# Kernel optimization log

Measured on AMD Instinct MI355X. Metric: run time of the kernel, lower is better.

The kernel has to match this reference:

```python
import jax, jax.numpy as jnp
import numpy as np
import math

D_MODEL = 1024
D_STATE = 16
D_CONV = 4
EXPAND = 2
D_INNER = EXPAND * D_MODEL
DT_RANK = max(D_MODEL // 16, 1)
B_SZ, L_SEQ = 2, 2048
DT_MIN, DT_MAX = 1e-3, 1e-1


def setup_inputs() -> dict:
    key = jax.random.key(0)
    ks = jax.random.split(key, 10)
    x = jax.random.normal(ks[0], (B_SZ, L_SEQ, D_MODEL), dtype=jnp.float32)
    # torch nn.Linear weights are [out, in]
    in_proj_w = jax.random.normal(ks[1], (2 * D_INNER, D_MODEL), jnp.float32) * 0.02
    conv_w = jax.random.normal(ks[2], (D_INNER, 1, D_CONV), jnp.float32) * 0.2  # depthwise [d,1,k]
    conv_b = jax.random.normal(ks[3], (D_INNER,), jnp.float32) * 0.02
    x_proj_w = jax.random.normal(ks[4], (DT_RANK + 2 * D_STATE, D_INNER), jnp.float32) * 0.02
    dt_init_std = DT_RANK ** -0.5
    dt_proj_w = jax.random.uniform(ks[5], (D_INNER, DT_RANK), jnp.float32, -dt_init_std, dt_init_std)
    dt = jnp.exp(jax.random.uniform(ks[6], (D_INNER,)) * (math.log(DT_MAX) - math.log(DT_MIN)) + math.log(DT_MIN))
    dt = jnp.clip(dt, DT_MIN, None)
    dt_proj_b = dt + jnp.log(-jnp.expm1(-dt))  # inverse softplus
    A = jnp.tile(jnp.arange(1, D_STATE + 1, dtype=jnp.float32)[None, :], (D_INNER, 1))
    A_log = jnp.log(A)
    D_param = jnp.ones((D_INNER,), jnp.float32)
    out_proj_w = jax.random.normal(ks[7], (D_MODEL, D_INNER), jnp.float32) * 0.02
    return {"x": x, "in_proj_w": in_proj_w, "conv_w": conv_w, "conv_b": conv_b,
            "x_proj_w": x_proj_w, "dt_proj_w": dt_proj_w, "dt_proj_b": dt_proj_b,
            "A_log": A_log, "D_param": D_param, "out_proj_w": out_proj_w}


def _ssm_forward(x, in_proj_w, conv_w, conv_b, x_proj_w, dt_proj_w, dt_proj_b, A_log, D_param, out_proj_w):
    B, L, _ = x.shape
    xz = jnp.einsum('bld,ed->ble', x, in_proj_w)          # [B,L,2*d_inner]
    x_branch, z = jnp.split(xz, 2, axis=-1)               # each [B,L,d_inner]
    # causal depthwise conv over L
    xc = jnp.transpose(x_branch, (0, 2, 1))               # [B,d,L]
    xc = jnp.pad(xc, ((0, 0), (0, 0), (D_CONV - 1, 0)))
    xc = jax.lax.conv_general_dilated(xc, conv_w, window_strides=(1,), padding='VALID',
                                      feature_group_count=D_INNER)
    xc = xc + conv_b[None, :, None]
    x_conv = jax.nn.silu(jnp.transpose(xc, (0, 2, 1)))    # [B,L,d_inner]
    # input-dependent projections
    xp = jnp.einsum('bld,ed->ble', x_conv, x_proj_w)      # [B,L,dt_rank+2n]
    dt_low, Bp, Cp = jnp.split(xp, [DT_RANK, DT_RANK + D_STATE], axis=-1)
    dt = jax.nn.softplus(jnp.einsum('blr,dr->bld', dt_low, dt_proj_w) + dt_proj_b)  # [B,L,d]
    A = -jnp.exp(A_log)                                   # [d,n]
    # sequential selective scan via lax.scan (time-major inputs)
    def step(h, inp):
        dt_t, B_t, C_t, x_t = inp                         # [B,d],[B,n],[B,n],[B,d]
        dA = jnp.exp(dt_t[:, :, None] * A[None])          # [B,d,n]
        h = dA * h + (dt_t * x_t)[:, :, None] * B_t[:, None, :]
        y = jnp.einsum('bdn,bn->bd', h, C_t)
        return h, y

    h0 = jnp.zeros((B, D_INNER, D_STATE), x.dtype)
    xs = (jnp.swapaxes(dt, 0, 1), jnp.swapaxes(Bp, 0, 1), jnp.swapaxes(Cp, 0, 1), jnp.swapaxes(x_conv, 0, 1))
    _, ys = jax.lax.scan(step, h0, xs)                    # ys: [L,B,d]
    y = jnp.swapaxes(ys, 0, 1)                            # [B,L,d]
    y = y + D_param * x_conv
    y = y * jax.nn.silu(z)
    return jnp.einsum('bld,ed->ble', y, out_proj_w)       # [B,L,d_model]


def reference(x, in_proj_w, conv_w, conv_b, x_proj_w, dt_proj_w, dt_proj_b, A_log, D_param, out_proj_w):
    return _ssm_forward(x, in_proj_w, conv_w, conv_b, x_proj_w, dt_proj_w, dt_proj_b, A_log, D_param, out_proj_w)
```

## Files before the change

### kernel.cpp

```cpp
#include <hip/hip_runtime.h>
#include <math.h>

#define BB      2
#define LSEQ    2048
#define DMODEL  1024
#define DINNER  2048
#define DSTATE  16
#define DTRANK  64
#define NPROJ   96
#define MROWS   (BB * LSEQ)
#define NCHUNK  64
#define CLEN    32
#define XKS     16

typedef unsigned short u16;
typedef short bf16x8 __attribute__((ext_vector_type(8)));
typedef float f32x4  __attribute__((ext_vector_type(4)));

struct HL { unsigned int hx, hy, lx, ly; };

__device__ __forceinline__ HL cvt4(float4 v) {
  unsigned int tx = __float_as_uint(v.x) & 0xFFFF0000u;
  unsigned int ty = __float_as_uint(v.y) & 0xFFFF0000u;
  unsigned int tz = __float_as_uint(v.z) & 0xFFFF0000u;
  unsigned int tw = __float_as_uint(v.w) & 0xFFFF0000u;
  HL r;
  r.hx = (tx >> 16) | ty;
  r.hy = (tz >> 16) | tw;
  float lx = v.x - __uint_as_float(tx);
  float ly = v.y - __uint_as_float(ty);
  float lz = v.z - __uint_as_float(tz);
  float lw = v.w - __uint_as_float(tw);
  unsigned int a = __float_as_uint(lx); a += 0x7FFFu + ((a >> 16) & 1u);
  unsigned int b = __float_as_uint(ly); b += 0x7FFFu + ((b >> 16) & 1u);
  unsigned int c = __float_as_uint(lz); c += 0x7FFFu + ((c >> 16) & 1u);
  unsigned int d = __float_as_uint(lw); d += 0x7FFFu + ((d >> 16) & 1u);
  r.lx = (a >> 16) | (b & 0xFFFF0000u);
  r.ly = (c >> 16) | (d & 0xFFFF0000u);
  return r;
}

__global__ __launch_bounds__(256)
void cvt_hl(const float4* __restrict__ src, uint2* __restrict__ dh,
            uint2* __restrict__ dl, int n4) {
  int i = blockIdx.x * 256 + threadIdx.x;
  if (i < n4) {
    HL r = cvt4(src[i]);
    dh[i] = make_uint2(r.hx, r.hy);
    dl[i] = make_uint2(r.lx, r.ly);
  }
}

__device__ __forceinline__ void gll16(const void* g, void* l) {
  __builtin_amdgcn_global_load_lds(
      (const __attribute__((address_space(1))) void*)g,
      (__attribute__((address_space(3))) void*)l, 16, 0, 0);
}

__global__ __launch_bounds__(512, 1)
void gemm_hl256(const u16* __restrict__ Ahp, const u16* __restrict__ Alp,
                const u16* __restrict__ Bhp, const u16* __restrict__ Blp,
                float* __restrict__ C0, float* __restrict__ C1,
                int M, int N, int K, int Nout, int XC_C) {
  __shared__ __align__(16) u16 L[2][4][256 * 32];

  const int tid = threadIdx.x;
  const int nbx = N >> 8, nby = M >> 8;
  const int xcd = blockIdx.x & 7;
  const int pos = blockIdx.x >> 3;
  const int cr = xcd / XC_C, cc = xcd - cr * XC_C;
  const int GCc = nbx / XC_C;
  const int GR  = (nby * XC_C) >> 3;
  const int by = cr * GR + pos / GCc;
  const int bx = cc * GCc + pos % GCc;
  const int row0 = by << 8, col0 = bx << 8;

  const int lane = tid & 63, w = tid >> 6;
  const int wr = w >> 2, wc = w & 3;
  const int fr = lane & 15, g = lane >> 4;
  const int lrow = lane >> 2, lslot = lane & 3;

  f32x4 acc[8][4] = {};
  const int NT = K >> 5;

#define STAGE256(pb, k0)                                                   \
  {                                                                        \
    _Pragma("unroll")                                                      \
    for (int s = 0; s < 2; ++s) {                                          \
      const int r = w * 32 + s * 16 + lrow;                                \
      const int csrc = (lslot ^ ((r >> 1) & 3)) << 3;                      \
      const size_t gA = (size_t)(row0 + r) * K + (k0) + csrc;              \
      const size_t gB = (size_t)(col0 + r) * K + (k0) + csrc;              \
      const int lb = w * 1024 + s * 512;                                   \
      gll16(Ahp + gA, &L[pb][0][lb]);                                      \
      gll16(Alp + gA, &L[pb][1][lb]);                                      \
      gll16(Bhp + gB, &L[pb][2][lb]);                                      \
      gll16(Blp + gB, &L[pb][3][lb]);                                      \
    }                                                                      \
  }

  STAGE256(0, 0);
  asm volatile("s_waitcnt vmcnt(0)" ::: "memory");
  __syncthreads();

  int p = 0;
  for (int t = 0; t < NT; ++t) {
    const bool pf = (t + 1 < NT);
    if (pf) STAGE256(p ^ 1, (t + 1) * 32);

    bf16x8 bh[4], bl[4];
#pragma unroll
    for (int j = 0; j < 4; ++j) {
      const int rb = wc * 64 + j * 16 + fr;
      const int o = rb * 32 + ((g ^ ((rb >> 1) & 3)) << 3);
      bh[j] = *(const bf16x8*)&L[p][2][o];
      bl[j] = *(const bf16x8*)&L[p][3][o];
    }
#pragma unroll
    for (int i = 0; i < 8; ++i) {
      const int ra = wr * 128 + i * 16 + fr;
      const int o = ra * 32 + ((g ^ ((ra >> 1) & 3)) << 3);
      bf16x8 ah = *(const bf16x8*)&L[p][0][o];
      bf16x8 al = *(const bf16x8*)&L[p][1][o];
#pragma unroll
      for (int j = 0; j < 4; ++j) {
        acc[i][j] = __builtin_amdgcn_mfma_f32_16x16x32_bf16(al, bh[j], acc[i][j], 0, 0, 0);
        acc[i][j] = __builtin_amdgcn_mfma_f32_16x16x32_bf16(ah, bl[j], acc[i][j], 0, 0, 0);
        acc[i][j] = __builtin_amdgcn_mfma_f32_16x16x32_bf16(ah, bh[j], acc[i][j], 0, 0, 0);
      }
    }
    if (pf) {
      asm volatile("s_waitcnt vmcnt(0)" ::: "memory");
      __syncthreads();
    }
    p ^= 1;
  }

  float* Cd;
  int cc0;
  if (C1 != nullptr && col0 >= Nout) { Cd = C1; cc0 = col0 - Nout; }
  else                               { Cd = C0; cc0 = col0; }
#pragma unroll
  for (int i = 0; i < 8; ++i) {
    const int rbase = row0 + wr * 128 + i * 16 + (lane >> 4) * 4;
#pragma unroll
    for (int j = 0; j < 4; ++j) {
      const int cfull = cc0 + wc * 64 + j * 16 + fr;
#pragma unroll
      for (int r = 0; r < 4; ++r)
        Cd[(size_t)(rbase + r) * Nout + cfull] = acc[i][j][r];
    }
  }
#undef STAGE256
}

__global__ __launch_bounds__(256, 3)
void gemm_hl(const u16* __restrict__ Ahp, const u16* __restrict__ Alp,
             const u16* __restrict__ Bhp, const u16* __restrict__ Blp,
             float* __restrict__ C0, float* __restrict__ C1,
             int M, int N, int K, int Nout, int XC_C) {
  __shared__ __align__(16) u16 L[4][128 * 32];

  const int tid = threadIdx.x;
  const int nbx = N >> 7, nby = M >> 7;
  const int xcd = blockIdx.x & 7;
  const int pos = blockIdx.x >> 3;
  const int cr = xcd / XC_C, cc = xcd - cr * XC_C;
  const int GCc = nbx / XC_C;
  const int GR  = (nby * XC_C) >> 3;
  const int by = cr * GR + pos / GCc;
  const int bx = cc * GCc + pos % GCc;
  const int row0 = by << 7, col0 = bx << 7;

  const int lane = tid & 63, w = tid >> 6;
  const int wr = w >> 1, wc = w & 1;
  const int fr = lane & 15, g = lane >> 4;
  const int lrow = lane >> 2, lslot = lane & 3;

  f32x4 acc[4][4] = {};

  for (int k0 = 0; k0 < K; k0 += 32) {
#pragma unroll
    for (int s = 0; s < 2; ++s) {
      const int r = w * 32 + s * 16 + lrow;
      const int csrc = (lslot ^ ((r >> 1) & 3)) << 3;
      const size_t gA = (size_t)(row0 + r) * K + k0 + csrc;
      const size_t gB = (size_t)(col0 + r) * K + k0 + csrc;
      const int lb = w * 1024 + s * 512;
      gll16(Ahp + gA, &L[0][lb]);
      gll16(Alp + gA, &L[1][lb]);
      gll16(Bhp + gB, &L[2][lb]);
      gll16(Blp + gB, &L[3][lb]);
    }
    __syncthreads();

    bf16x8 bh[4], bl[4];
#pragma unroll
    for (int j = 0; j < 4; ++j) {
      const int rb = wc * 64 + j * 16 + fr;
      const int o = rb * 32 + ((g ^ ((rb >> 1) & 3)) << 3);
      bh[j] = *(const bf16x8*)&L[2][o];
      bl[j] = *(const bf16x8*)&L[3][o];
    }
#pragma unroll
    for (int i = 0; i < 4; ++i) {
      const int ra = wr * 64 + i * 16 + fr;
      const int o = ra * 32 + ((g ^ ((ra >> 1) & 3)) << 3);
      bf16x8 ah = *(const bf16x8*)&L[0][o];
      bf16x8 al = *(const bf16x8*)&L[1][o];
#pragma unroll
      for (int j = 0; j < 4; ++j) {
        acc[i][j] = __builtin_amdgcn_mfma_f32_16x16x32_bf16(al, bh[j], acc[i][j], 0, 0, 0);
        acc[i][j] = __builtin_amdgcn_mfma_f32_16x16x32_bf16(ah, bl[j], acc[i][j], 0, 0, 0);
        acc[i][j] = __builtin_amdgcn_mfma_f32_16x16x32_bf16(ah, bh[j], acc[i][j], 0, 0, 0);
      }
    }
    __syncthreads();
  }

  float* Cd;
  int cc0;
  if (C1 != nullptr && col0 >= Nout) { Cd = C1; cc0 = col0 - Nout; }
  else                               { Cd = C0; cc0 = col0; }
#pragma unroll
  for (int i = 0; i < 4; ++i) {
    const int rbase = row0 + wr * 64 + i * 16 + (lane >> 4) * 4;
#pragma unroll
    for (int j = 0; j < 4; ++j) {
      const int cfull = cc0 + wc * 64 + j * 16 + fr;
#pragma unroll
      for (int r = 0; r < 4; ++r)
        Cd[(size_t)(rbase + r) * Nout + cfull] = acc[i][j][r];
    }
  }
}

template <int ACT>
__global__ __launch_bounds__(256)
void gemm_tn(const float* __restrict__ A, const float* __restrict__ B,
             float* __restrict__ C, const float* __restrict__ bias,
             int M, int N, int K, int lda) {
  __shared__ float As[8][128];
  __shared__ float Bs[8][128];
  const int tid  = threadIdx.x;
  const int row0 = blockIdx.y * 128;
  const int col0 = blockIdx.x * 128;
  const int tx = tid & 15, ty = tid >> 4;
  const int lr = tid >> 1;
  const int lk = (tid & 1) * 4;

  float acc[8][8];
#pragma unroll
  for (int i = 0; i < 8; ++i)
#pragma unroll
    for (int j = 0; j < 8; ++j) acc[i][j] = 0.f;

  const float* Aptr = A + (size_t)(row0 + lr) * lda + lk;
  const int bcol = col0 + lr;
  const float* Bptr = (bcol < N) ? (B + (size_t)bcol * K + lk) : nullptr;

  float4 av = *(const float4*)(Aptr);
  float4 bv = Bptr ? *(const float4*)(Bptr) : make_float4(0.f, 0.f, 0.f, 0.f);

  for (int k0 = 0; k0 < K; k0 += 8) {
    As[lk + 0][lr] = av.x; As[lk + 1][lr] = av.y;
    As[lk + 2][lr] = av.z; As[lk + 3][lr] = av.w;
    Bs[lk + 0][lr] = bv.x; Bs[lk + 1][lr] = bv.y;
    Bs[lk + 2][lr] = bv.z; Bs[lk + 3][lr] = bv.w;
    if (k0 + 8 < K) {
      av = *(const float4*)(Aptr + k0 + 8);
      if (Bptr) bv = *(const float4*)(Bptr + k0 + 8);
    }
    __syncthreads();
#pragma unroll
    for (int k = 0; k < 8; ++k) {
      float a[8], b[8];
      *(float4*)&a[0] = *(const float4*)&As[k][ty * 4];
      *(float4*)&a[4] = *(const float4*)&As[k][64 + ty * 4];
      *(float4*)&b[0] = *(const float4*)&Bs[k][tx * 4];
      *(float4*)&b[4] = *(const float4*)&Bs[k][64 + tx * 4];
#pragma unroll
      for (int i = 0; i < 8; ++i)
#pragma unroll
        for (int j = 0; j < 8; ++j)
          acc[i][j] = fmaf(a[i], b[j], acc[i][j]);
    }
    __syncthreads();
  }

#pragma unroll
  for (int ih = 0; ih < 2; ++ih) {
#pragma unroll
    for (int i2 = 0; i2 < 4; ++i2) {
      int r = row0 + ih * 64 + ty * 4 + i2;
      if (r >= M) continue;
#pragma unroll
      for (int jh = 0; jh < 2; ++jh) {
        int c = col0 + jh * 64 + tx * 4;
        float vv[4];
#pragma unroll
        for (int j = 0; j < 4; ++j) {
          float v = acc[ih * 4 + i2][jh * 4 + j];
          if (ACT == 1) {
            v += bias[c + j];
            v = (v > 20.f) ? v : log1pf(expf(v));
          }
          vv[j] = v;
        }
        if (c + 3 < N) {
          *(float4*)(C + (size_t)r * N + c) = make_float4(vv[0], vv[1], vv[2], vv[3]);
        } else {
          for (int j = 0; j < 4; ++j)
            if (c + j < N) C[(size_t)r * N + c + j] = vv[j];
        }
      }
    }
  }
}

__global__ __launch_bounds__(256)
void xproj_splitk(const float* __restrict__ A, const float* __restrict__ W,
                  float* __restrict__ Pq) {
  __shared__ float As[8][128];
  __shared__ float Ws[8][96];
  const int tid  = threadIdx.x;
  const int row0 = blockIdx.x * 128;
  const int k0b  = blockIdx.y * (DINNER / XKS);
  const int tx = tid & 15, ty = tid >> 4;
  const int lr = tid >> 1, lk = (tid & 1) * 4;

  float acc[8][6];
#pragma unroll
  for (int i = 0; i < 8; ++i)
#pragma unroll
    for (int j = 0; j < 6; ++j) acc[i][j] = 0.f;

  const float* Ap = A + (size_t)(row0 + lr) * DINNER + lk;
  const float* Wp = (tid < 192) ? (W + (size_t)(tid >> 1) * DINNER + (tid & 1) * 4)
                                : nullptr;
  float4 av = *(const float4*)(Ap + k0b);
  float4 wv = Wp ? *(const float4*)(Wp + k0b) : make_float4(0.f, 0.f, 0.f, 0.f);

  for (int k0 = k0b; k0 < k0b + DINNER / XKS; k0 += 8) {
    As[lk + 0][lr] = av.x; As[lk + 1][lr] = av.y;
    As[lk + 2][lr] = av.z; As[lk + 3][lr] = av.w;
    if (Wp) {
      int j = tid >> 1, kk = (tid & 1) * 4;
      Ws[kk + 0][j] = wv.x; Ws[kk + 1][j] = wv.y;
      Ws[kk + 2][j] = wv.z; Ws[kk + 3][j] = wv.w;
    }
    if (k0 + 8 < k0b + DINNER / XKS) {
      av = *(const float4*)(Ap + k0 + 8);
      if (Wp) wv = *(const float4*)(Wp + k0 + 8);
    }
    __syncthreads();
#pragma unroll
    for (int kk = 0; kk < 8; ++kk) {
      float a[8], w[6];
      *(float4*)&a[0] = *(const float4*)&As[kk][ty * 8];
      *(float4*)&a[4] = *(const float4*)&As[kk][ty * 8 + 4];
#pragma unroll
      for (int j = 0; j < 6; ++j) w[j] = Ws[kk][tx * 6 + j];
#pragma unroll
      for (int i = 0; i < 8; ++i)
#pragma unroll
        for (int j = 0; j < 6; ++j)
          acc[i][j] = fmaf(a[i], w[j], acc[i][j]);
    }
    __syncthreads();
  }
  float* dst = Pq + (size_t)blockIdx.y * (MROWS * NPROJ);
#pragma unroll
  for (int i = 0; i < 8; ++i)
#pragma unroll
    for (int j = 0; j < 6; ++j)
      dst[(size_t)(row0 + ty * 8 + i) * NPROJ + tx * 6 + j] = acc[i][j];
}

__global__ __launch_bounds__(256)
void xpj_reduce(const float* __restrict__ Pq, float* __restrict__ xpb) {
  int idx = blockIdx.x * 256 + threadIdx.x;
  float s = 0.f;
#pragma unroll
  for (int q = 0; q < XKS; ++q)
    s += Pq[(size_t)q * (MROWS * NPROJ) + idx];
  xpb[idx] = s;
}

__global__ __launch_bounds__(256)
void conv_silu_kernel(const float* __restrict__ xb, const float* __restrict__ cw,
                      const float* __restrict__ cb, float* __restrict__ xc) {
  int idx = (blockIdx.x * 256 + threadIdx.x) * 4;
  int d  = idx & (DINNER - 1);
  int ml = idx >> 11;
  int l  = ml & (LSEQ - 1);
  float4 W0 = *(const float4*)(cw + (d + 0) * 4);
  float4 W1 = *(const float4*)(cw + (d + 1) * 4);
  float4 W2 = *(const float4*)(cw + (d + 2) * 4);
  float4 W3 = *(const float4*)(cw + (d + 3) * 4);
  const float* base = xb + (size_t)ml * DINNER + d;
  float4 z4 = make_float4(0.f, 0.f, 0.f, 0.f);
  float4 r0  = *(const float4*)(base);
  float4 rm1 = (l >= 1) ? *(const float4*)(base - DINNER)     : z4;
  float4 rm2 = (l >= 2) ? *(const float4*)(base - 2 * DINNER) : z4;
  float4 rm3 = (l >= 3) ? *(const float4*)(base - 3 * DINNER) : z4;
  float4 bias = *(const float4*)(cb + d);
  float4 o;
  o.x = bias.x + r0.x * W0.w + rm1.x * W0.z + rm2.x * W0.y + rm3.x * W0.x;
  o.y = bias.y + r0.y * W1.w + rm1.y * W1.z + rm2.y * W1.y + rm3.y * W1.x;
  o.z = bias.z + r0.z * W2.w + rm1.z * W2.z + rm2.z * W2.y + rm3.z * W2.x;
  o.w = bias.w + r0.w * W3.w + rm1.w * W3.z + rm2.w * W3.y + rm3.w * W3.x;
  o.x = o.x / (1.f + expf(-o.x));
  o.y = o.y / (1.f + expf(-o.y));
  o.z = o.z / (1.f + expf(-o.z));
  o.w = o.w / (1.f + expf(-o.w));
  *(float4*)(xc + idx) = o;
}

__global__ __launch_bounds__(256)
void scan_chunk_kernel(const float* __restrict__ dt, const float* __restrict__ xp,
                       const float* __restrict__ xc, const float* __restrict__ A_log,
                       float* __restrict__ P, float* __restrict__ H) {
  __shared__ float sbc[CLEN][32];
  const int tid = threadIdx.x;
  const int bid = blockIdx.x;
  const int b  = bid >> 9;
  const int c  = (bid >> 3) & 63;
  const int dg = bid & 7;
  const int d  = dg * 256 + tid;
  const int m0 = b * LSEQ + c * CLEN;
  {
    int r = tid >> 3, q = (tid & 7) * 4;
    *(float4*)&sbc[r][q] = *(const float4*)(xp + (size_t)(m0 + r) * NPROJ + DTRANK + q);
  }
  float a2[DSTATE], h[DSTATE];
#pragma unroll
  for (int n = 0; n < DSTATE; ++n) {
    a2[n] = -expf(A_log[d * DSTATE + n]) * 1.44269504f;
    h[n] = 0.f;
  }
  float dtsum = 0.f;
  __syncthreads();

  const float* dtp = dt + (size_t)m0 * DINNER + d;
  const float* xcp = xc + (size_t)m0 * DINNER + d;
  float ndt = dtp[0], nxc = xcp[0];
  for (int s = 0; s < CLEN; ++s) {
    float dtv = ndt, xv = nxc;
    int sp = (s + 1 < CLEN) ? s + 1 : s;
    ndt = dtp[(size_t)sp * DINNER];
    nxc = xcp[(size_t)sp * DINNER];
    dtsum += dtv;
    float dtx = dtv * xv;
    float Bv[16];
    *(float4*)&Bv[0]  = *(const float4*)&sbc[s][0];
    *(float4*)&Bv[4]  = *(const float4*)&sbc[s][4];
    *(float4*)&Bv[8]  = *(const float4*)&sbc[s][8];
    *(float4*)&Bv[12] = *(const float4*)&sbc[s][12];
#pragma unroll
    for (int n = 0; n < DSTATE; ++n) {
      float a = exp2f(dtv * a2[n]);
      h[n] = fmaf(a, h[n], dtx * Bv[n]);
    }
  }
  size_t o = ((size_t)(b * NCHUNK + c) * DINNER + d) * DSTATE;
  float4* Hp = (float4*)(H + o);
  Hp[0] = make_float4(h[0], h[1], h[2], h[3]);
  Hp[1] = make_float4(h[4], h[5], h[6], h[7]);
  Hp[2] = make_float4(h[8], h[9], h[10], h[11]);
  Hp[3] = make_float4(h[12], h[13], h[14], h[15]);
  float p[16];
#pragma unroll
  for (int n = 0; n < DSTATE; ++n) p[n] = exp2f(a2[n] * dtsum);
  float4* Pp = (float4*)(P + o);
  Pp[0] = make_float4(p[0], p[1], p[2], p[3]);
  Pp[1] = make_float4(p[4], p[5], p[6], p[7]);
  Pp[2] = make_float4(p[8], p[9], p[10], p[11]);
  Pp[3] = make_float4(p[12], p[13], p[14], p[15]);
}

__global__ __launch_bounds__(256)
void stitch_kernel(const float* __restrict__ P, float* __restrict__ H) {
  int idx = blockIdx.x * 256 + threadIdx.x;
  int b = idx >> 15, e = idx & 32767;
  size_t base = (size_t)b * NCHUNK * 32768 + e;
  float h = 0.f;
  for (int c = 0; c < NCHUNK; ++c) {
    size_t o = base + (size_t)c * 32768;
    float p = P[o], q = H[o];
    H[o] = h;
    h = fmaf(p, h, q);
  }
}

__global__ __launch_bounds__(256)
void scan_out_kernel(const float* dt, const float* __restrict__ xp,
                     const float* __restrict__ xc, const float* __restrict__ z,
                     const float* __restrict__ A_log, const float* __restrict__ Dp,
                     const float* __restrict__ Hinit, float* y) {
  __shared__ float sbc[CLEN][32];
  const int tid = threadIdx.x;
  const int bid = blockIdx.x;
  const int b  = bid >> 9;
  const int c  = (bid >> 3) & 63;
  const int dg = bid & 7;
  const int d  = dg * 256 + tid;
  const int m0 = b * LSEQ + c * CLEN;
  {
    int r = tid >> 3, q = (tid & 7) * 4;
    *(float4*)&sbc[r][q] = *(const float4*)(xp + (size_t)(m0 + r) * NPROJ + DTRANK + q);
  }
  float a2[DSTATE], h[DSTATE];
  size_t ho = ((size_t)(b * NCHUNK + c) * DINNER + d) * DSTATE;
  const float4* Hp = (const float4*)(Hinit + ho);
  float4 h0 = Hp[0], h1 = Hp[1], h2 = Hp[2], h3 = Hp[3];
  h[0]=h0.x; h[1]=h0.y; h[2]=h0.z; h[3]=h0.w;
  h[4]=h1.x; h[5]=h1.y; h[6]=h1.z; h[7]=h1.w;
  h[8]=h2.x; h[9]=h2.y; h[10]=h2.z; h[11]=h2.w;
  h[12]=h3.x; h[13]=h3.y; h[14]=h3.z; h[15]=h3.w;
#pragma unroll
  for (int n = 0; n < DSTATE; ++n)
    a2[n] = -expf(A_log[d * DSTATE + n]) * 1.44269504f;
  const float Dv = Dp[d];
  __syncthreads();

  const float* dtp = dt + (size_t)m0 * DINNER + d;
  const float* xcp = xc + (size_t)m0 * DINNER + d;
  const float* zp  = z  + (size_t)m0 * DINNER + d;
  float* yp = y + (size_t)m0 * DINNER + d;
  float ndt = dtp[0], nxc = xcp[0], nz = zp[0];
  for (int s = 0; s < CLEN; ++s) {
    float dtv = ndt, xv = nxc, zv = nz;
    int sp = (s + 1 < CLEN) ? s + 1 : s;
    ndt = dtp[(size_t)sp * DINNER];
    nxc = xcp[(size_t)sp * DINNER];
    nz  = zp[(size_t)sp * DINNER];
    float dtx = dtv * xv;
    float Bv[16], Cv[16];
    *(float4*)&Bv[0]  = *(const float4*)&sbc[s][0];
    *(float4*)&Bv[4]  = *(const float4*)&sbc[s][4];
    *(float4*)&Bv[8]  = *(const float4*)&sbc[s][8];
    *(float4*)&Bv[12] = *(const float4*)&sbc[s][12];
    *(float4*)&Cv[0]  = *(const float4*)&sbc[s][16];
    *(float4*)&Cv[4]  = *(const float4*)&sbc[s][20];
    *(float4*)&Cv[8]  = *(const float4*)&sbc[s][24];
    *(float4*)&Cv[12] = *(const float4*)&sbc[s][28];
    float yv = 0.f;
#pragma unroll
    for (int n = 0; n < DSTATE; ++n) {
      float a = exp2f(dtv * a2[n]);
      h[n] = fmaf(a, h[n], dtx * Bv[n]);
      yv = fmaf(h[n], Cv[n], yv);
    }
    yv = (yv + Dv * xv) * (zv / (1.f + expf(-zv)));
    yp[(size_t)s * DINNER] = yv;
  }
}

extern "C" void kernel_launch(void* const* d_in, const int* in_sizes, int n_in,
                              void* d_out, int out_size, void* d_ws, size_t ws_size,
                              hipStream_t stream) {
  const float* x          = (const float*)d_in[0];
  const float* in_proj_w  = (const float*)d_in[1];
  const float* conv_w     = (const float*)d_in[2];
  const float* conv_b     = (const float*)d_in[3];
  const float* x_proj_w   = (const float*)d_in[4];
  const float* dt_proj_w  = (const float*)d_in[5];
  const float* dt_proj_b  = (const float*)d_in[6];
  const float* A_log      = (const float*)d_in[7];
  const float* D_param    = (const float*)d_in[8];
  const float* out_proj_w = (const float*)d_in[9];
  float* out = (float*)d_out;
  float* ws  = (float*)d_ws;

  float* xb   = ws;
  float* dtr  = xb;
  float* zb   = ws + 8388608;
  float* xcb  = ws + 16777216;
  float* xpb  = ws + 25165824;
  float* Pbuf = ws + 25559040;
  float* Hbuf = ws + 29753344;
  float* Pq   = Pbuf;

  u16* xh = (u16*)(ws + 16777216);
  u16* xl = (u16*)(ws + 16777216 + 2097152);
  u16* wh = (u16*)(ws + 16777216 + 4194304);
  u16* wl = (u16*)(ws + 16777216 + 6291456);
  u16* yh = (u16*)(ws + 16777216);
  u16* yl = (u16*)(ws + 16777216 + 4194304);
  u16* oh = (u16*)(ws + 25559040);
  u16* ol = (u16*)(ws + 25559040 + 1048576);

  dim3 blk(256);
  cvt_hl<<<4096, blk, 0, stream>>>((const float4*)x, (uint2*)xh, (uint2*)xl, 1048576);
  cvt_hl<<<4096, blk, 0, stream>>>((const float4*)in_proj_w, (uint2*)wh, (uint2*)wl, 1048576);
  gemm_hl256<<<dim3((MROWS / 256) * (2 * DINNER / 256)), dim3(512), 0, stream>>>(
      xh, xl, wh, wl, xb, zb, MROWS, 2 * DINNER, DMODEL, DINNER, 4);
  conv_silu_kernel<<<(MROWS * DINNER) / 1024, blk, 0, stream>>>(xb, conv_w, conv_b, xcb);
  xproj_splitk<<<dim3(MROWS / 128, XKS), blk, 0, stream>>>(xcb, x_proj_w, Pq);
  xpj_reduce<<<(MROWS * NPROJ) / 256, blk, 0, stream>>>(Pq, xpb);
  gemm_tn<1><<<dim3(DINNER / 128, MROWS / 128), blk, 0, stream>>>(
      xpb, dt_proj_w, dtr, dt_proj_b, MROWS, DINNER, DTRANK, NPROJ);
  scan_chunk_kernel<<<dim3(BB * NCHUNK * 8), blk, 0, stream>>>(
      dtr, xpb, xcb, A_log, Pbuf, Hbuf);
  stitch_kernel<<<dim3(BB * DINNER * DSTATE / 256), blk, 0, stream>>>(Pbuf, Hbuf);
  scan_out_kernel<<<dim3(BB * NCHUNK * 8), blk, 0, stream>>>(
      dtr, xpb, xcb, zb, A_log, D_param, Hbuf, xb);
  cvt_hl<<<8192, blk, 0, stream>>>((const float4*)xb, (uint2*)yh, (uint2*)yl, 2097152);
  cvt_hl<<<2048, blk, 0, stream>>>((const float4*)out_proj_w, (uint2*)oh, (uint2*)ol, 524288);
  gemm_hl<<<dim3((MROWS / 128) * (DMODEL / 128)), blk, 0, stream>>>(
      yh, yl, oh, ol, out, out, MROWS, DMODEL, DINNER, DMODEL, 1);
}
```

Measured before the change: 499.5 us.

## Merge paired conversion launches and restructure GEMM inner loop with barriers and priority

Two pairs of fp32-to-bf16 hi/lo conversion launches are merged into single launches, removing two kernel launches. In the 256-tile split-bf16 GEMM, all A fragments are now loaded from LDS up front and the loop iterates over B columns, with s_barrier and s_setprio around each MFMA group so waves interleave LDS reads and matrix work. __syncthreads is replaced by raw s_barrier. The extra barriers per k-step can add stalls, and holding more A fragments live raises register pressure.

```diff
diff --git a/kernel.cpp b/kernel.cpp
--- a/kernel.cpp
+++ b/kernel.cpp
@@ -41,13 +41,20 @@
 }
 
 __global__ __launch_bounds__(256)
-void cvt_hl(const float4* __restrict__ src, uint2* __restrict__ dh,
-            uint2* __restrict__ dl, int n4) {
+void cvt_hl2(const float4* __restrict__ s0, uint2* __restrict__ h0,
+             uint2* __restrict__ l0, int n0,
+             const float4* __restrict__ s1, uint2* __restrict__ h1,
+             uint2* __restrict__ l1, int n1) {
   int i = blockIdx.x * 256 + threadIdx.x;
-  if (i < n4) {
-    HL r = cvt4(src[i]);
-    dh[i] = make_uint2(r.hx, r.hy);
-    dl[i] = make_uint2(r.lx, r.ly);
+  if (i < n0) {
+    HL r = cvt4(s0[i]);
+    h0[i] = make_uint2(r.hx, r.hy);
+    l0[i] = make_uint2(r.lx, r.ly);
+  } else if (i - n0 < n1) {
+    int j = i - n0;
+    HL r = cvt4(s1[j]);
+    h1[j] = make_uint2(r.hx, r.hy);
+    l1[j] = make_uint2(r.lx, r.ly);
   }
 }
 
@@ -101,37 +108,43 @@
 
   STAGE256(0, 0);
   asm volatile("s_waitcnt vmcnt(0)" ::: "memory");
-  __syncthreads();
+  __builtin_amdgcn_s_barrier();
 
   int p = 0;
   for (int t = 0; t < NT; ++t) {
     const bool pf = (t + 1 < NT);
     if (pf) STAGE256(p ^ 1, (t + 1) * 32);
 
-    bf16x8 bh[4], bl[4];
+    bf16x8 ah[8], al[8];
+#pragma unroll
+    for (int i = 0; i < 8; ++i) {
+      const int ra = wr * 128 + i * 16 + fr;
+      const int o = ra * 32 + ((g ^ ((ra >> 1) & 3)) << 3);
+      ah[i] = *(const bf16x8*)&L[p][0][o];
+      al[i] = *(const bf16x8*)&L[p][1][o];
+    }
+
 #pragma unroll
     for (int j = 0; j < 4; ++j) {
       const int rb = wc * 64 + j * 16 + fr;
       const int o = rb * 32 + ((g ^ ((rb >> 1) & 3)) << 3);
-      bh[j] = *(const bf16x8*)&L[p][2][o];
-      bl[j] = *(const bf16x8*)&L[p][3][o];
-    }
-#pragma unroll
-    for (int i = 0; i < 8; ++i) {
-      const int ra = wr * 128 + i * 16 + fr;
-      const int o = ra * 32 + ((g ^ ((ra >> 1) & 3)) << 3);
-      bf16x8 ah = *(const bf16x8*)&L[p][0][o];
-      bf16x8 al = *(const bf16x8*)&L[p][1][o];
-#pragma unroll
-      for (int j = 0; j < 4; ++j) {
-        acc[i][j] = __builtin_amdgcn_mfma_f32_16x16x32_bf16(al, bh[j], acc[i][j], 0, 0, 0);
-        acc[i][j] = __builtin_amdgcn_mfma_f32_16x16x32_bf16(ah, bl[j], acc[i][j], 0, 0, 0);
-        acc[i][j] = __builtin_amdgcn_mfma_f32_16x16x32_bf16(ah, bh[j], acc[i][j], 0, 0, 0);
+      bf16x8 bh = *(const bf16x8*)&L[p][2][o];
+      bf16x8 bl = *(const bf16x8*)&L[p][3][o];
+      __builtin_amdgcn_s_barrier();
+      __builtin_amdgcn_s_setprio(1);
+#pragma unroll
+      for (int i = 0; i < 8; ++i) {
+        acc[i][j] = __builtin_amdgcn_mfma_f32_16x16x32_bf16(al[i], bh, acc[i][j], 0, 0, 0);
+        acc[i][j] = __builtin_amdgcn_mfma_f32_16x16x32_bf16(ah[i], bl, acc[i][j], 0, 0, 0);
+        acc[i][j] = __builtin_amdgcn_mfma_f32_16x16x32_bf16(ah[i], bh, acc[i][j], 0, 0, 0);
       }
-    }
+      __builtin_amdgcn_s_setprio(0);
+      __builtin_amdgcn_s_barrier();
+    }
+
     if (pf) {
       asm volatile("s_waitcnt vmcnt(0)" ::: "memory");
-      __syncthreads();
+      __builtin_amdgcn_s_barrier();
     }
     p ^= 1;
   }
@@ -592,8 +605,9 @@
   u16* ol = (u16*)(ws + 25559040 + 1048576);
 
   dim3 blk(256);
-  cvt_hl<<<4096, blk, 0, stream>>>((const float4*)x, (uint2*)xh, (uint2*)xl, 1048576);
-  cvt_hl<<<4096, blk, 0, stream>>>((const float4*)in_proj_w, (uint2*)wh, (uint2*)wl, 1048576);
+  cvt_hl2<<<8192, blk, 0, stream>>>(
+      (const float4*)x, (uint2*)xh, (uint2*)xl, 1048576,
+      (const float4*)in_proj_w, (uint2*)wh, (uint2*)wl, 1048576);
   gemm_hl256<<<dim3((MROWS / 256) * (2 * DINNER / 256)), dim3(512), 0, stream>>>(
       xh, xl, wh, wl, xb, zb, MROWS, 2 * DINNER, DMODEL, DINNER, 4);
   conv_silu_kernel<<<(MROWS * DINNER) / 1024, blk, 0, stream>>>(xb, conv_w, conv_b, xcb);
@@ -606,8 +620,9 @@
   stitch_kernel<<<dim3(BB * DINNER * DSTATE / 256), blk, 0, stream>>>(Pbuf, Hbuf);
   scan_out_kernel<<<dim3(BB * NCHUNK * 8), blk, 0, stream>>>(
       dtr, xpb, xcb, zb, A_log, D_param, Hbuf, xb);
-  cvt_hl<<<8192, blk, 0, stream>>>((const float4*)xb, (uint2*)yh, (uint2*)yl, 2097152);
-  cvt_hl<<<2048, blk, 0, stream>>>((const float4*)out_proj_w, (uint2*)oh, (uint2*)ol, 524288);
+  cvt_hl2<<<10240, blk, 0, stream>>>(
+      (const float4*)xb, (uint2*)yh, (uint2*)yl, 2097152,
+      (const float4*)out_proj_w, (uint2*)oh, (uint2*)ol, 524288);
   gemm_hl<<<dim3((MROWS / 128) * (DMODEL / 128)), blk, 0, stream>>>(
       yh, yl, oh, ol, out, out, MROWS, DMODEL, DINNER, DMODEL, 1);
 }
```

Measured after the change: 504.8 us. Within noise of the previous version (+1.1%).
